# Kernel tuning notes

Measured on AMD Instinct MI355X. Metric: run time of the kernel, lower is better.

The kernel has to match this reference:

```python
import jax, jax.numpy as jnp
import numpy as np
import math

V, D, H, DFF, NL, CTX = 32000, 512, 8, 2048, 2, 1024
B, S = 2, 1024

def ln(x, w, eps=1e-5):
    mu = jnp.mean(x, axis=-1, keepdims=True)
    var = jnp.var(x, axis=-1, keepdims=True)
    return (x - mu) / jnp.sqrt(var + eps) * w

def setup_inputs() -> dict:
    key = jax.random.key(0)
    ks = jax.random.split(key, 10)
    inp = {
        "x": jax.random.randint(ks[0], (B, S), 0, V),
        "wte": jax.random.normal(ks[1], (V, D), jnp.float32) * 0.02,
        "wpe": jax.random.normal(ks[2], (CTX + 1, D), jnp.float32) * 0.02,
        "ln_e_w": jnp.ones((D,), jnp.float32),
        "ln_p_w": jnp.ones((D,), jnp.float32),
        "ln_f_w": jnp.ones((D,), jnp.float32),
        "ln_mlp_w": jnp.ones((D,), jnp.float32),
        "W_q_diag": jax.random.normal(ks[3], (H, D), jnp.float32) * 0.02,
        "W_k_diag": jax.random.normal(ks[4], (H, D), jnp.float32) * 0.02,
        "W_o": jax.random.normal(ks[5], (NL, D, D * H), jnp.float32) * (0.02 / math.sqrt(2 * NL)),
        "mlp_w1": jax.random.normal(ks[6], (DFF, D), jnp.float32) * 0.02,
        "mlp_w2": jax.random.normal(ks[7], (D, DFF), jnp.float32) * 0.02,
    }
    return inp

def reference(x, wte, wpe, ln_e_w, ln_p_w, ln_f_w, ln_mlp_w, W_q_diag, W_k_diag, W_o, mlp_w1, mlp_w2):
    Bsz, Sl = x.shape
    e = ln(wte[x], ln_e_w)                       # (B,S,D)
    p = ln(wpe[: Sl + 1], ln_p_w)                # (S+1,D), identical across batch
    Q = p[1:][None, :, :] * W_q_diag[:, None, :]   # (H,S,D)
    K = p[:-1][None, :, :] * W_k_diag[:, None, :]  # (H,S,D)
    krn = jnp.einsum('hsd,htd->hst', Q, K) / math.sqrt(D)
    mask = jnp.tril(jnp.ones((Sl, Sl), bool))
    krn = jnp.where(mask[None], krn, 0.0)        # (H,S,S)
    wn = 1.0 / (jnp.arange(Sl, dtype=jnp.float32) + 1.0)  # W_N diagonal

    f_k = jnp.zeros_like(e)
    for i in range(NL):
        # R = softmax over S of (V,D)@(B,D,S) -> (B,V,S)
        R = jax.nn.softmax(jnp.einsum('vd,bsd->bvs', wte, f_k), axis=-1)
        ex_wte = jnp.einsum('bvs,vd->bsd', R, wte)
        ex_wte = ex_wte / jnp.sum(R, axis=1)[..., None]  # normalize by sum over V
        Vt = e - ex_wte                                   # (B,S,D)
        delta = jnp.einsum('hst,btd->bhsd', krn, Vt)      # (B,H,S,D)
        delta = delta * wn[None, None, :, None]           # W_N row scaling
        delta = jnp.transpose(delta, (0, 2, 1, 3)).reshape(Bsz, Sl, H * D)
        delta = delta @ W_o[i].T                          # (B,S,D)
        f_k = f_k + delta
        # use_ff MLP block
        h = ln(f_k, ln_mlp_w)
        f_k = f_k + jax.nn.gelu(h @ mlp_w1.T, approximate=False) @ mlp_w2.T

    out = ln(f_k, ln_f_w)
    logits = out[:, -1:, :] @ wte.T               # (B,1,V), targets=None branch
    return logits
```

## Files before the change

kernel.cpp:

```cpp
#include <hip/hip_runtime.h>

#define DV   512
#define SV   1024
#define BV   2
#define VV   32000
#define HV   8
#define DFFV 2048
#define NLV  2
#define KCX  25

typedef __bf16 bf16;
typedef __bf16 bf16x4 __attribute__((ext_vector_type(4)));
typedef __bf16 bf16x8 __attribute__((ext_vector_type(8)));
typedef float  f32x4  __attribute__((ext_vector_type(4)));

__device__ __forceinline__ void lds_dma16(const void* g, void* l) {
  __builtin_amdgcn_global_load_lds(
      (const __attribute__((address_space(1))) unsigned int*)g,
      (__attribute__((address_space(3))) unsigned int*)l,
      16, 0, 0);
}

template<typename OUT>
__device__ __forceinline__ void row_ln_512(const float* __restrict__ src,
                                           const float* __restrict__ w,
                                           OUT* __restrict__ dst, int lane) {
  const float4 a = *(const float4*)(src + lane*8);
  const float4 b = *(const float4*)(src + lane*8 + 4);
  float s = a.x+a.y+a.z+a.w + b.x+b.y+b.z+b.w;
  float q = a.x*a.x+a.y*a.y+a.z*a.z+a.w*a.w + b.x*b.x+b.y*b.y+b.z*b.z+b.w*b.w;
#pragma unroll
  for (int off = 32; off > 0; off >>= 1) {
    s += __shfl_down(s, off, 64);
    q += __shfl_down(q, off, 64);
  }
  s = __shfl(s, 0, 64); q = __shfl(q, 0, 64);
  const float mu   = s * (1.0f/512.0f);
  const float rstd = rsqrtf(q * (1.0f/512.0f) - mu*mu + 1e-5f);
  const float4 wa = *(const float4*)(w + lane*8);
  const float4 wb = *(const float4*)(w + lane*8 + 4);
  OUT* d = dst + lane*8;
  d[0] = (OUT)((a.x-mu)*rstd*wa.x);
  d[1] = (OUT)((a.y-mu)*rstd*wa.y);
  d[2] = (OUT)((a.z-mu)*rstd*wa.z);
  d[3] = (OUT)((a.w-mu)*rstd*wa.w);
  d[4] = (OUT)((b.x-mu)*rstd*wb.x);
  d[5] = (OUT)((b.y-mu)*rstd*wb.y);
  d[6] = (OUT)((b.z-mu)*rstd*wb.z);
  d[7] = (OUT)((b.w-mu)*rstd*wb.w);
}

__global__ void embed_wpe_ln_k(const int* __restrict__ x, const float* __restrict__ wte,
                               const float* __restrict__ wpe, const float* __restrict__ we,
                               const float* __restrict__ wp, float* __restrict__ e,
                               float* __restrict__ pn) {
  const int row = blockIdx.x * 4 + (threadIdx.x >> 6);
  const int lane = threadIdx.x & 63;
  if (row < BV*SV) {
    row_ln_512<float>(wte + (long)x[row] * DV, we, e + (long)row * DV, lane);
  } else {
    const int r = row - BV*SV;
    if (r >= SV + 1) return;
    row_ln_512<float>(wpe + (long)r * DV, wp, pn + (long)r * DV, lane);
  }
}

__global__ void cast3_f2b_k(const float* __restrict__ Wo, const float* __restrict__ w1,
                            const float* __restrict__ w2, bf16* __restrict__ Wob,
                            bf16* __restrict__ w1b, bf16* __restrict__ w2b) {
  const long n0 = (long)NLV*DV*HV*DV, n1 = (long)DFFV*DV, n2 = (long)DV*DFFV;
  long i = ((long)blockIdx.x * 256 + threadIdx.x) * 4;
  const float* in; bf16* o; long r;
  if (i < n0)            { in = Wo; o = Wob; r = i; }
  else if (i < n0 + n1)  { in = w1; o = w1b; r = i - n0; }
  else if (i < n0+n1+n2) { in = w2; o = w2b; r = i - n0 - n1; }
  else return;
  const float4 v = *(const float4*)(in + r);
  bf16x4 ob; ob[0]=(bf16)v.x; ob[1]=(bf16)v.y; ob[2]=(bf16)v.z; ob[3]=(bf16)v.w;
  *(bf16x4*)(&o[r]) = ob;
}

__global__ void wte_prep_k(const float* __restrict__ wte, bf16* __restrict__ wb,
                           bf16* __restrict__ wbT, float* __restrict__ wm) {
  __shared__ float t[32][33];
  __shared__ float cpart[8][32];
  const int d0 = blockIdx.x * 32, v0 = blockIdx.y * 32;
  const int tx = threadIdx.x, ty = threadIdx.y;
  float csum = 0.f;
#pragma unroll
  for (int k = 0; k < 4; k++) {
    const int vl = ty*4 + k;
    const float val = wte[(long)(v0+vl)*DV + d0+tx];
    t[vl][tx] = val;
    csum += val;
  }
  cpart[ty][tx] = csum;
  __syncthreads();
  const int tid = ty*32 + tx;
  const int r = tid >> 3, c = (tid & 7) * 4;
  {
    bf16x4 o;
    o[0] = (bf16)t[r][c];   o[1] = (bf16)t[r][c+1];
    o[2] = (bf16)t[r][c+2]; o[3] = (bf16)t[r][c+3];
    *(bf16x4*)(&wb[(long)(v0+r)*DV + d0+c]) = o;
  }
  {
    bf16x4 o;
    o[0] = (bf16)t[c][r];   o[1] = (bf16)t[c+1][r];
    o[2] = (bf16)t[c+2][r]; o[3] = (bf16)t[c+3][r];
    *(bf16x4*)(&wbT[(long)(d0+r)*VV + v0+c]) = o;
  }
  if (ty == 0) {
    float s = 0.f;
#pragma unroll
    for (int k = 0; k < 8; k++) s += cpart[k][tx];
    atomicAdd(&wm[d0+tx], s);
  }
}

__global__ void qk_prep_k(const float* __restrict__ pn, const float* __restrict__ Wq,
                          const float* __restrict__ Wk, bf16* __restrict__ Qh,
                          bf16* __restrict__ Kh) {
  const int s = blockIdx.x, hh = blockIdx.y;
  const int d = threadIdx.x * 4;
  const float4 q  = *(const float4*)(pn + (long)(s+1)*DV + d);
  const float4 kk = *(const float4*)(pn + (long)s*DV + d);
  const float4 aq = *(const float4*)(Wq + (long)hh*DV + d);
  const float4 ak = *(const float4*)(Wk + (long)hh*DV + d);
  const long o = ((long)hh*SV + s)*DV + d;
  Qh[o+0]=(bf16)(q.x*aq.x);  Qh[o+1]=(bf16)(q.y*aq.y);
  Qh[o+2]=(bf16)(q.z*aq.z);  Qh[o+3]=(bf16)(q.w*aq.w);
  Kh[o+0]=(bf16)(kk.x*ak.x); Kh[o+1]=(bf16)(kk.y*ak.y);
  Kh[o+2]=(bf16)(kk.z*ak.z); Kh[o+3]=(bf16)(kk.w*ak.w);
}

__global__ void freduce_ln_k(const float* __restrict__ part, float* __restrict__ f_k,
                             const float* __restrict__ w, bf16* __restrict__ hbuf,
                             int KC, int init) {
  const int row = blockIdx.x * 4 + (threadIdx.x >> 6);
  const int lane = threadIdx.x & 63;
  const int b = row >> 10;
  const long ro = (long)row * DV + lane*8;
  const long po = (long)(row & (SV-1)) * DV + lane*8;
  float v[8];
  if (init) {
#pragma unroll
    for (int k = 0; k < 8; k++) v[k] = 0.f;
  } else {
    const float4 a = *(const float4*)(f_k + ro);
    const float4 c = *(const float4*)(f_k + ro + 4);
    v[0]=a.x;v[1]=a.y;v[2]=a.z;v[3]=a.w;v[4]=c.x;v[5]=c.y;v[6]=c.z;v[7]=c.w;
  }
  for (int c = 0; c < KC; c++) {
    const float* pp = part + ((long)(b*KC + c))*SV*DV + po;
    const float4 a = *(const float4*)pp;
    const float4 d = *(const float4*)(pp + 4);
    v[0]+=a.x;v[1]+=a.y;v[2]+=a.z;v[3]+=a.w;v[4]+=d.x;v[5]+=d.y;v[6]+=d.z;v[7]+=d.w;
  }
  { float4 o1={v[0],v[1],v[2],v[3]}, o2={v[4],v[5],v[6],v[7]};
    *(float4*)(f_k + ro) = o1; *(float4*)(f_k + ro + 4) = o2; }
  float s = 0.f, q = 0.f;
#pragma unroll
  for (int k = 0; k < 8; k++) { s += v[k]; q += v[k]*v[k]; }
#pragma unroll
  for (int off = 32; off > 0; off >>= 1) {
    s += __shfl_down(s, off, 64);
    q += __shfl_down(q, off, 64);
  }
  s = __shfl(s, 0, 64); q = __shfl(q, 0, 64);
  const float mu   = s * (1.0f/512.0f);
  const float rstd = rsqrtf(q * (1.0f/512.0f) - mu*mu + 1e-5f);
  const float4 wa = *(const float4*)(w + lane*8);
  const float4 wb = *(const float4*)(w + lane*8 + 4);
  bf16* d = hbuf + (long)row * DV + lane*8;
  d[0] = (bf16)((v[0]-mu)*rstd*wa.x);
  d[1] = (bf16)((v[1]-mu)*rstd*wa.y);
  d[2] = (bf16)((v[2]-mu)*rstd*wa.z);
  d[3] = (bf16)((v[3]-mu)*rstd*wa.w);
  d[4] = (bf16)((v[4]-mu)*rstd*wb.x);
  d[5] = (bf16)((v[5]-mu)*rstd*wb.y);
  d[6] = (bf16)((v[6]-mu)*rstd*wb.z);
  d[7] = (bf16)((v[7]-mu)*rstd*wb.w);
}

__global__ void freduce_cast_k(const float* __restrict__ part, float* __restrict__ f_k,
                               bf16* __restrict__ fb, int KC, int do_cast) {
  const long i = ((long)blockIdx.x * 256 + threadIdx.x) * 4;
  const int  b = (int)(i / ((long)SV*DV));
  const long r = i % ((long)SV*DV);
  float4 acc = *(const float4*)(f_k + i);
  for (int c = 0; c < KC; c++) {
    const float4 v = *(const float4*)(part + ((long)(b*KC + c))*SV*DV + r);
    acc.x += v.x; acc.y += v.y; acc.z += v.z; acc.w += v.w;
  }
  *(float4*)(f_k + i) = acc;
  if (do_cast) {
    bf16x4 o; o[0]=(bf16)acc.x; o[1]=(bf16)acc.y; o[2]=(bf16)acc.z; o[3]=(bf16)acc.w;
    *(bf16x4*)(&fb[i]) = o;
  }
}

__global__ void vt_part_k(const float* __restrict__ e, const bf16* __restrict__ pb,
                          const float* __restrict__ part, bf16* __restrict__ VtT) {
  __shared__ float t[32][33];
  __shared__ float cpart[8][32];
  __shared__ float csum[32];
  const int d0 = blockIdx.x * 32, s0 = blockIdx.y * 32;
  const int tx = threadIdx.x, ty = threadIdx.y;
  {
    float cs = 0.f;
    for (int v = ty; v < VV/128; v += 8) cs += part[(long)v * SV + s0 + tx];
    cpart[ty][tx] = cs;
  }
  __syncthreads();
  if (ty == 0) {
    float s = 0.f;
#pragma unroll
    for (int k = 0; k < 8; k++) s += cpart[k][tx];
    csum[tx] = s;
  }
  __syncthreads();
#pragma unroll
  for (int k = 0; k < 4; k++) {
    const int sl = ty + k*8;
    const long off = (long)(s0+sl)*DV + d0+tx;
    float acc = 0.f;
    for (int c = 0; c < KCX; c++) acc += (float)pb[(long)c*SV*DV + off];
    t[sl][tx] = e[off] - acc / csum[sl];
  }
  __syncthreads();
#pragma unroll
  for (int k = 0; k < 4; k++) {
    const int dl = ty + k*8;
    VtT[(long)(d0+dl)*SV + s0+tx] = (bf16)t[tx][dl];
  }
}

__global__ void vt0_transpose_k(const float* __restrict__ e, const float* __restrict__ wm,
                                bf16* __restrict__ VtT) {
  __shared__ float t[32][33];
  const int d0 = blockIdx.x * 32, s0 = blockIdx.y * 32, b = blockIdx.z;
  const int tx = threadIdx.x, ty = threadIdx.y;
  const float* eb = e + (long)b*SV*DV;
  bf16* vb = VtT + (long)b*DV*SV;
  const float mval = wm[d0 + tx] * (1.0f / (float)VV);
#pragma unroll
  for (int k = 0; k < 4; k++) {
    const int sl = ty + k*8;
    t[sl][tx] = eb[(long)(s0+sl)*DV + d0+tx] - mval;
  }
  __syncthreads();
#pragma unroll
  for (int k = 0; k < 4; k++) {
    const int dl = ty + k*8;
    vb[(long)(d0+dl)*SV + s0+tx] = (bf16)t[tx][dl];
  }
}


__global__ void u_last_k(const bf16* __restrict__ krn, const bf16* __restrict__ VtT,
                         bf16* __restrict__ u) {
  const int wv = threadIdx.x >> 6, lane = threadIdx.x & 63;
  const int d = blockIdx.x * 4 + wv;
  const int h = blockIdx.y, b = blockIdx.z;
  const bf16* kr = krn + (long)h*SV*SV + (long)(SV-1)*SV;
  const bf16* vr = VtT + (long)b*DV*SV + (long)d*SV;
  float acc = 0.f;
#pragma unroll
  for (int it = 0; it < 2; it++) {
    const int k = lane*8 + it*512;
    const bf16x8 a = *(const bf16x8*)(kr + k);
    const bf16x8 v = *(const bf16x8*)(vr + k);
#pragma unroll
    for (int i = 0; i < 8; i++) acc += (float)a[i] * (float)v[i];
  }
#pragma unroll
  for (int off = 32; off > 0; off >>= 1) acc += __shfl_down(acc, off, 64);
  if (lane == 0) u[((long)b*HV + h)*DV + d] = (bf16)acc;
}

template<int ACT>
__global__ void gemv_k(const bf16* __restrict__ W, const bf16* __restrict__ vec,
                       float* __restrict__ outf, bf16* __restrict__ outb,
                       int M, int K, long sVb) {
  const int wv = threadIdx.x >> 6, lane = threadIdx.x & 63;
  const int m = blockIdx.x * 4 + wv;
  const int b = blockIdx.y;
  if (m >= M) return;
  const bf16* wr = W + (long)m * K;
  const bf16* vb = vec + (long)b * sVb;
  float acc = 0.f;
  for (int k = lane*8; k < K; k += 512) {
    const bf16x8 a = *(const bf16x8*)(wr + k);
    const bf16x8 v = *(const bf16x8*)(vb + k);
#pragma unroll
    for (int i = 0; i < 8; i++) acc += (float)a[i] * (float)v[i];
  }
#pragma unroll
  for (int off = 32; off > 0; off >>= 1) acc += __shfl_down(acc, off, 64);
  if (lane == 0) {
    if (ACT == 0) outf[(long)b * M + m] = acc;
    else {
      const float ge = 0.5f * acc * (1.0f + erff(acc * 0.70710678118f));
      outb[(long)b * M + m] = (bf16)ge;
    }
  }
}

__global__ void mid_ln_k(const float* __restrict__ f_k, const float* __restrict__ delta,
                         const float* __restrict__ w, float* __restrict__ f_last,
                         bf16* __restrict__ h) {
  const int b = threadIdx.x >> 6;
  if (b >= BV) return;
  const int lane = threadIdx.x & 63;
  const long ro = ((long)b * SV + (SV - 1)) * DV + lane*8;
  const float* dp = delta + (long)b * DV + lane*8;
  float v[8];
  { const float4 a = *(const float4*)(f_k + ro);
    const float4 c = *(const float4*)(f_k + ro + 4);
    const float4 da = *(const float4*)dp;
    const float4 db = *(const float4*)(dp + 4);
    v[0]=a.x+da.x; v[1]=a.y+da.y; v[2]=a.z+da.z; v[3]=a.w+da.w;
    v[4]=c.x+db.x; v[5]=c.y+db.y; v[6]=c.z+db.z; v[7]=c.w+db.w; }
  { float* fl = f_last + (long)b*DV + lane*8;
    float4 o1={v[0],v[1],v[2],v[3]}, o2v={v[4],v[5],v[6],v[7]};
    *(float4*)fl = o1; *(float4*)(fl+4) = o2v; }
  float s = 0.f, q = 0.f;
#pragma unroll
  for (int k = 0; k < 8; k++) { s += v[k]; q += v[k]*v[k]; }
#pragma unroll
  for (int off = 32; off > 0; off >>= 1) {
    s += __shfl_down(s, off, 64);
    q += __shfl_down(q, off, 64);
  }
  s = __shfl(s, 0, 64); q = __shfl(q, 0, 64);
  const float mu   = s * (1.0f/512.0f);
  const float rstd = rsqrtf(q * (1.0f/512.0f) - mu*mu + 1e-5f);
  const float4 wa = *(const float4*)(w + lane*8);
  const float4 wb = *(const float4*)(w + lane*8 + 4);
  bf16* d = h + (long)b * DV + lane*8;
  d[0] = (bf16)((v[0]-mu)*rstd*wa.x);
  d[1] = (bf16)((v[1]-mu)*rstd*wa.y);
  d[2] = (bf16)((v[2]-mu)*rstd*wa.z);
  d[3] = (bf16)((v[3]-mu)*rstd*wa.w);
  d[4] = (bf16)((v[4]-mu)*rstd*wb.x);
  d[5] = (bf16)((v[5]-mu)*rstd*wb.y);
  d[6] = (bf16)((v[6]-mu)*rstd*wb.z);
  d[7] = (bf16)((v[7]-mu)*rstd*wb.w);
}

__global__ void final2_k(const float* __restrict__ f_last, const float* __restrict__ o2,
                         const float* __restrict__ w, float* __restrict__ obuf) {
  const int b = threadIdx.x >> 6;
  if (b >= BV) return;
  const int lane = threadIdx.x & 63;
  const float* fl = f_last + (long)b * DV + lane*8;
  const float* op = o2 + (long)b * DV + lane*8;
  float v[8];
  { const float4 a = *(const float4*)fl;
    const float4 c = *(const float4*)(fl + 4);
    const float4 da = *(const float4*)op;
    const float4 db = *(const float4*)(op + 4);
    v[0]=a.x+da.x; v[1]=a.y+da.y; v[2]=a.z+da.z; v[3]=a.w+da.w;
    v[4]=c.x+db.x; v[5]=c.y+db.y; v[6]=c.z+db.z; v[7]=c.w+db.w; }
  float s = 0.f, q = 0.f;
#pragma unroll
  for (int k = 0; k < 8; k++) { s += v[k]; q += v[k]*v[k]; }
#pragma unroll
  for (int off = 32; off > 0; off >>= 1) {
    s += __shfl_down(s, off, 64);
    q += __shfl_down(q, off, 64);
  }
  s = __shfl(s, 0, 64); q = __shfl(q, 0, 64);
  const float mu   = s * (1.0f/512.0f);
  const float rstd = rsqrtf(q * (1.0f/512.0f) - mu*mu + 1e-5f);
  const float4 wa = *(const float4*)(w + lane*8);
  const float4 wb = *(const float4*)(w + lane*8 + 4);
  float* d = obuf + (long)b * DV + lane*8;
  d[0] = (v[0]-mu)*rstd*wa.x;
  d[1] = (v[1]-mu)*rstd*wa.y;
  d[2] = (v[2]-mu)*rstd*wa.z;
  d[3] = (v[3]-mu)*rstd*wa.w;
  d[4] = (v[4]-mu)*rstd*wb.x;
  d[5] = (v[5]-mu)*rstd*wb.y;
  d[6] = (v[6]-mu)*rstd*wb.z;
  d[7] = (v[7]-mu)*rstd*wb.w;
}

__global__ void logits_k(const float* __restrict__ obuf, const float* __restrict__ wte,
                         float* __restrict__ out, int V) {
  const int wv = threadIdx.x >> 6, lane = threadIdx.x & 63;
  const int v = blockIdx.x * 4 + wv;
  const float* wr = wte + (long)v * DV;
  const float4 a  = *(const float4*)(wr + lane*8);
  const float4 c  = *(const float4*)(wr + lane*8 + 4);
  const float4 oa0 = *(const float4*)(obuf + lane*8);
  const float4 ob0 = *(const float4*)(obuf + lane*8 + 4);
  const float4 oa1 = *(const float4*)(obuf + DV + lane*8);
  const float4 ob1 = *(const float4*)(obuf + DV + lane*8 + 4);
  float d0 = a.x*oa0.x + a.y*oa0.y + a.z*oa0.z + a.w*oa0.w
           + c.x*ob0.x + c.y*ob0.y + c.z*ob0.z + c.w*ob0.w;
  float d1 = a.x*oa1.x + a.y*oa1.y + a.z*oa1.z + a.w*oa1.w
           + c.x*ob1.x + c.y*ob1.y + c.z*ob1.z + c.w*ob1.w;
#pragma unroll
  for (int off = 32; off > 0; off >>= 1) {
    d0 += __shfl_down(d0, off, 64);
    d1 += __shfl_down(d1, off, 64);
  }
  if (lane == 0) { out[v] = d0; out[(long)V + v] = d1; }
}

__device__ __forceinline__ long xcd_swz(long lin, long nwg) {
  const long qq = nwg >> 3, rr = nwg & 7;
  const long xcd = lin & 7, idx = lin >> 3;
  return (xcd < rr ? xcd * (qq + 1) : rr * (qq + 1) + (xcd - rr) * qq) + idx;
}

struct GemmArgs {
  const bf16* A; const bf16* B;
  float* Cf; bf16* Cb;
  int K, lda, ldb, ldc;
  long sAh, sAb, sBh, sBb, sCh, sCb;
  int Hmod, KC, causal, swap;
  float scale;
};

template<int EPI>
__global__ __launch_bounds__(256)
void gemm_nt(GemmArgs g) {
  __shared__ bf16 As[2][128*32];
  __shared__ bf16 Bs[2][128*32];
  const int tid = threadIdx.x;
  int bx = blockIdx.x, by = blockIdx.y, z = blockIdx.z;
  {
    const int nbx = gridDim.x, nby = gridDim.y;
    const long nwg = (long)nbx * nby * gridDim.z;
    long lin = xcd_swz(bx + (long)nbx * (by + (long)nby * z), nwg);
    bx = (int)(lin % nbx);
    const long t2 = lin / nbx;
    by = (int)(t2 % nby);
    z  = (int)(t2 / nby);
  }
  const int chunk = z % g.KC;
  const int zo = z / g.KC;
  const int h = zo % g.Hmod;
  const int b = zo / g.Hmod;
  if (g.swap) { int t = bx; bx = by; by = t; }
  const int m0 = by * 128;
  const int n0 = bx * 128;
  const long coff = (long)h * g.sCh + (long)b * g.sCb;

  if (EPI == 3 && n0 > m0 + 127) return;

  const bf16* A = g.A + (long)h * g.sAh + (long)b * g.sAb;
  const bf16* B = g.B + (long)h * g.sBh + (long)b * g.sBb;
  const int lane = tid & 63;
  const int wv = tid >> 6;
  const int wm = (wv >> 1) * 64;
  const int wn = (wv & 1) * 64;
  const int frow = lane & 15;
  const int quad = lane >> 4;
  const int sg8  = ((lane & 3) ^ ((lane >> 3) & 3)) * 8;
  const int drow = lane >> 2;

  const f32x4 fzero = {0.f, 0.f, 0.f, 0.f};
  f32x4 acc[4][4];
#pragma unroll
  for (int i = 0; i < 4; i++)
#pragma unroll
    for (int j = 0; j < 4; j++) acc[i][j] = fzero;

  int k0, klen;
  if (g.causal) { k0 = 0; klen = min(g.K, m0 + 128); }
  else          { klen = g.K / g.KC; k0 = chunk * klen; }

  auto stage = [&](int buf, int kk) {
#pragma unroll
    for (int c = 0; c < 2; c++) {
      const int rb = c*64 + wv*16;
      lds_dma16(A + (long)(m0 + rb + drow) * g.lda + kk + sg8, &As[buf][rb*32]);
      lds_dma16(B + (long)(n0 + rb + drow) * g.ldb + kk + sg8, &Bs[buf][rb*32]);
    }
  };

  const int nsteps = klen >> 5;
  int cur = 0;
  stage(0, k0);
  for (int it = 0; it < nsteps; ++it) {
    if (it + 1 < nsteps) {
      stage(cur ^ 1, k0 + (it + 1) * 32);
      asm volatile("s_waitcnt vmcnt(4)" ::: "memory");
    } else {
      asm volatile("s_waitcnt vmcnt(0)" ::: "memory");
    }
    __builtin_amdgcn_s_barrier();
    bf16x8 af[4], bfr[4];
    const int sw = (frow >> 1) & 3;
#pragma unroll
    for (int i = 0; i < 4; i++)
      af[i] = *(const bf16x8*)(&As[cur][(wm + i*16 + frow)*32 + ((quad ^ sw))*8]);
#pragma unroll
    for (int j = 0; j < 4; j++)
      bfr[j] = *(const bf16x8*)(&Bs[cur][(wn + j*16 + frow)*32 + ((quad ^ sw))*8]);
#pragma unroll
    for (int i = 0; i < 4; i++)
#pragma unroll
      for (int j = 0; j < 4; j++)
        acc[i][j] = __builtin_amdgcn_mfma_f32_16x16x32_bf16(af[i], bfr[j], acc[i][j], 0, 0, 0);
    __builtin_amdgcn_s_barrier();
    cur ^= 1;
  }

  const int rb = quad * 4;
#pragma unroll
  for (int i = 0; i < 4; i++) {
#pragma unroll
    for (int j = 0; j < 4; j++) {
#pragma unroll
      for (int r = 0; r < 4; r++) {
        const int gm = m0 + wm + i*16 + rb + r;
        const int gn = n0 + wn + j*16 + frow;
        const float v = acc[i][j][r];
        if (EPI == 2) {
          g.Cb[coff + (long)gm * g.ldc + gn] = (bf16)v;
        } else if (EPI == 3) {
          const float val = (gn <= gm) ? v * g.scale / (float)(gm + 1) : 0.0f;
          g.Cb[coff + (long)gm * g.ldc + gn] = (bf16)val;
        } else if (EPI == 4) {
          const float ge = 0.5f * v * (1.0f + erff(v * 0.70710678118f));
          g.Cb[coff + (long)gm * g.ldc + gn] = (bf16)ge;
        } else if (EPI == 6) {
          g.Cf[(long)(b*g.KC + chunk) * g.sCh + (long)gm * g.ldc + gn] = v;
        }
      }
    }
  }
}

template<int EPI>
__global__ __launch_bounds__(512)
void gemm256(GemmArgs g) {
  __shared__ bf16 As[2][256*64];
  __shared__ bf16 Bs[2][256*64];
  const int tid = threadIdx.x;
  int bm = blockIdx.x, bn = blockIdx.y, z = blockIdx.z;
  {
    const int nbx = gridDim.x, nby = gridDim.y;
    const long nwg = (long)nbx * nby * gridDim.z;
    long lin = xcd_swz(bm + (long)nbx * (bn + (long)nby * z), nwg);
    bm = (int)(lin % nbx);
    const long t2 = lin / nbx;
    bn = (int)(t2 % nby);
    z  = (int)(t2 / nby);
  }
  const int m0 = bm * 256, n0 = bn * 256;
  const int lane = tid & 63, wv = tid >> 6;
  const int wm = (wv >> 2) * 128, wn = (wv & 3) * 64;
  const int frow = lane & 15, quad = lane >> 4;
  const int sg8  = ((lane & 7) ^ (lane >> 3)) * 8;
  const int drow = lane >> 3;

  const f32x4 fzero = {0.f, 0.f, 0.f, 0.f};
  f32x4 acc[8][4];
#pragma unroll
  for (int i = 0; i < 8; i++)
#pragma unroll
    for (int j = 0; j < 4; j++) acc[i][j] = fzero;

  const int klen = g.K / g.KC;
  const int k0 = z * klen;

  auto stage = [&](int buf, int kk) {
#pragma unroll
    for (int c = 0; c < 4; c++) {
      const int rb = c*64 + wv*8;
      lds_dma16(g.A + (long)(m0 + rb + drow) * g.lda + kk + sg8, &As[buf][rb*64]);
      lds_dma16(g.B + (long)(n0 + rb + drow) * g.ldb + kk + sg8, &Bs[buf][rb*64]);
    }
  };

  const int nsteps = klen >> 6;
  int cur = 0;
  stage(0, k0);
  for (int it = 0; it < nsteps; ++it) {
    if (it + 1 < nsteps) {
      stage(cur ^ 1, k0 + (it + 1) * 64);
      asm volatile("s_waitcnt vmcnt(8)" ::: "memory");
    } else {
      asm volatile("s_waitcnt vmcnt(0)" ::: "memory");
    }
    __builtin_amdgcn_s_barrier();
    const int sw = frow & 7;
#pragma unroll
    for (int ks = 0; ks < 2; ks++) {
      bf16x8 af[8], bfr[4];
#pragma unroll
      for (int j = 0; j < 4; j++)
        bfr[j] = *(const bf16x8*)(&Bs[cur][(wn + j*16 + frow)*64 + (((ks*4 + quad) ^ sw))*8]);
#pragma unroll
      for (int i = 0; i < 8; i++)
        af[i] = *(const bf16x8*)(&As[cur][(wm + i*16 + frow)*64 + (((ks*4 + quad) ^ sw))*8]);
#pragma unroll
      for (int i = 0; i < 8; i++)
#pragma unroll
        for (int j = 0; j < 4; j++)
          acc[i][j] = __builtin_amdgcn_mfma_f32_16x16x32_bf16(af[i], bfr[j], acc[i][j], 0, 0, 0);
    }
    __builtin_amdgcn_s_barrier();
    cur ^= 1;
  }

  const int rb4 = quad * 4;
  if (EPI == 5) {
    const int vblk = (n0 + wn) >> 7;
#pragma unroll
    for (int i = 0; i < 8; i++) {
#pragma unroll
      for (int r = 0; r < 4; r++) {
        const int gm = m0 + wm + i*16 + rb4 + r;
        float rs = 0.f;
#pragma unroll
        for (int j = 0; j < 4; j++) {
          const int gn = n0 + wn + j*16 + frow;
          const float ev = __expf(acc[i][j][r]);
          g.Cb[(long)gm * g.ldc + gn] = (bf16)ev;
          rs += ev;
        }
#pragma unroll
        for (int off = 1; off < 16; off <<= 1)
          rs += __shfl_xor(rs, off, 64);
        if (frow == 0) atomicAdd(g.Cf + (long)vblk * SV + gm, rs);
      }
    }
  } else {
#pragma unroll
    for (int i = 0; i < 8; i++) {
#pragma unroll
      for (int j = 0; j < 4; j++) {
#pragma unroll
        for (int r = 0; r < 4; r++) {
          const int gm = m0 + wm + i*16 + rb4 + r;
          const int gn = n0 + wn + j*16 + frow;
          g.Cb[(long)z * g.sCh + (long)gm * g.ldc + gn] = (bf16)acc[i][j][r];
        }
      }
    }
  }
}

static void layer_tail0(bf16* krn, bf16* VtT, bf16* U_rs, bf16* Wo_b,
                        float* f_k, bf16* f_k_b, bf16* hbuf, bf16* Gbuf, float* fpart,
                        bf16* w1_b, bf16* w2_b, const float* lnmw, hipStream_t stream) {
  {
    GemmArgs g = {};
    g.A = krn; g.B = VtT; g.Cb = U_rs;
    g.K = SV; g.lda = SV; g.ldb = SV; g.ldc = HV*DV;
    g.sAh = (long)SV*SV; g.sBb = (long)DV*SV;
    g.sCh = DV; g.sCb = (long)SV*HV*DV;
    g.Hmod = HV; g.KC = 1; g.causal = 1;
    gemm_nt<2><<<dim3(DV/128, SV/128, BV*HV), 256, 0, stream>>>(g);
  }
  {
    GemmArgs g = {};
    g.A = U_rs; g.B = Wo_b; g.Cf = fpart;
    g.K = HV*DV; g.lda = HV*DV; g.ldb = HV*DV; g.ldc = DV;
    g.sAb = (long)SV*HV*DV; g.sCh = (long)SV*DV;
    g.Hmod = 1; g.KC = 8; g.causal = 0;
    gemm_nt<6><<<dim3(DV/128, SV/128, BV*8), 256, 0, stream>>>(g);
  }
  freduce_ln_k<<<dim3(BV*SV/4), 256, 0, stream>>>(fpart, f_k, lnmw, hbuf, 8, 1);
  {
    GemmArgs g = {};
    g.A = hbuf; g.B = w1_b; g.Cb = Gbuf;
    g.K = DV; g.lda = DV; g.ldb = DV; g.ldc = DFFV;
    g.sAb = (long)SV*DV; g.sCb = (long)SV*DFFV;
    g.Hmod = 1; g.KC = 1; g.causal = 0;
    gemm_nt<4><<<dim3(DFFV/128, SV/128, BV), 256, 0, stream>>>(g);
  }
  {
    GemmArgs g = {};
    g.A = Gbuf; g.B = w2_b; g.Cf = fpart;
    g.K = DFFV; g.lda = DFFV; g.ldb = DFFV; g.ldc = DV;
    g.sAb = (long)SV*DFFV; g.sCh = (long)SV*DV;
    g.Hmod = 1; g.KC = 8; g.causal = 0;
    gemm_nt<6><<<dim3(DV/128, SV/128, BV*8), 256, 0, stream>>>(g);
  }
  freduce_cast_k<<<dim3(BV*SV*DV/4/256), 256, 0, stream>>>(fpart, f_k, f_k_b, 8, 1);
}

extern "C" void kernel_launch(void* const* d_in, const int* in_sizes, int n_in,
                              void* d_out, int out_size, void* d_ws, size_t ws_size,
                              hipStream_t stream) {
  const int*   x    = (const int*)d_in[0];
  const float* wte  = (const float*)d_in[1];
  const float* wpe  = (const float*)d_in[2];
  const float* lnew = (const float*)d_in[3];
  const float* lnpw = (const float*)d_in[4];
  const float* lnfw = (const float*)d_in[5];
  const float* lnmw = (const float*)d_in[6];
  const float* Wq   = (const float*)d_in[7];
  const float* Wk   = (const float*)d_in[8];
  const float* Wo   = (const float*)d_in[9];
  const float* w1   = (const float*)d_in[10];
  const float* w2   = (const float*)d_in[11];
  float* out = (float*)d_out;
  (void)in_sizes; (void)n_in; (void)out_size; (void)ws_size;

  char* p = (char*)d_ws;
  auto alloc = [&](size_t bytes) -> void* {
    void* r = (void*)p;
    p += (bytes + 255) & ~(size_t)255;
    return r;
  };
  float* e      = (float*)alloc((size_t)BV*SV*DV*4);
  float* pn     = (float*)alloc((size_t)(SV+1)*DV*4);
  bf16*  wteT_b = (bf16*)alloc((size_t)DV*VV*2);
  bf16*  wte_b  = (bf16*)alloc((size_t)VV*DV*2);
  bf16*  krn    = (bf16*)alloc((size_t)HV*SV*SV*2);
  bf16*  Wo_b   = (bf16*)alloc((size_t)NLV*DV*HV*DV*2);
  bf16*  w1_b   = (bf16*)alloc((size_t)DFFV*DV*2);
  bf16*  w2_b   = (bf16*)alloc((size_t)DV*DFFV*2);
  float* f_k    = (float*)alloc((size_t)BV*SV*DV*4);
  bf16*  f_k_b  = (bf16*)alloc((size_t)BV*SV*DV*2);
  bf16*  expart = (bf16*)alloc((size_t)KCX*SV*DV*2);
  bf16*  VtT    = (bf16*)alloc((size_t)BV*DV*SV*2);
  bf16*  hbuf   = (bf16*)alloc((size_t)BV*SV*DV*2);
  float* part   = (float*)alloc((size_t)BV*(VV/128)*SV*4);
  float* obuf   = (float*)alloc((size_t)BV*DV*4);
  float* wmean  = (float*)alloc((size_t)DV*4);
  bf16*  u_last = (bf16*)alloc((size_t)BV*HV*DV*2);
  float* delta  = (float*)alloc((size_t)BV*DV*4);
  float* f_last = (float*)alloc((size_t)BV*DV*4);
  bf16*  h_last = (bf16*)alloc((size_t)BV*DV*2);
  bf16*  g_last = (bf16*)alloc((size_t)BV*DFFV*2);
  float* o2buf  = (float*)alloc((size_t)BV*DV*4);
  char*  arena  = (char*)alloc((size_t)SV*VV*2);
  bf16*  Qh     = (bf16*)arena;
  bf16*  Kh     = (bf16*)(arena + (size_t)HV*SV*DV*2);
  bf16*  PT     = (bf16*)arena;
  bf16*  U_rs   = (bf16*)arena;
  bf16*  Gbuf   = (bf16*)(arena + (size_t)BV*SV*HV*DV*2);
  float* fpart  = (float*)(arena + (size_t)BV*SV*HV*DV*2 + (size_t)BV*SV*DFFV*2);

  hipMemsetAsync(wmean, 0, (size_t)DV*4, stream);
  hipMemsetAsync(part, 0, (size_t)BV*(VV/128)*SV*4, stream);
  wte_prep_k<<<dim3(DV/32, VV/32), dim3(32,8), 0, stream>>>(wte, wte_b, wteT_b, wmean);
  cast3_f2b_k<<<dim3((NLV*DV*HV*DV + DFFV*DV + DV*DFFV)/4/256), 256, 0, stream>>>(
      Wo, w1, w2, Wo_b, w1_b, w2_b);
  embed_wpe_ln_k<<<dim3((BV*SV + SV+1 + 3)/4), 256, 0, stream>>>(
      x, wte, wpe, lnew, lnpw, e, pn);
  qk_prep_k<<<dim3(SV, HV), 128, 0, stream>>>(pn, Wq, Wk, Qh, Kh);

  {
    GemmArgs g = {};
    g.A = Qh; g.B = Kh; g.Cb = krn;
    g.K = DV; g.lda = DV; g.ldb = DV; g.ldc = SV;
    g.sAh = (long)SV*DV; g.sBh = (long)SV*DV; g.sCh = (long)SV*SV;
    g.Hmod = HV; g.KC = 1; g.causal = 0;
    g.scale = 0.044194173824159216f;
    gemm_nt<3><<<dim3(SV/128, SV/128, HV), 256, 0, stream>>>(g);
  }

  vt0_transpose_k<<<dim3(DV/32, SV/32, BV), dim3(32,8), 0, stream>>>(e, wmean, VtT);
  layer_tail0(krn, VtT, U_rs, Wo_b, f_k, f_k_b, hbuf, Gbuf, fpart,
              w1_b, w2_b, lnmw, stream);

  for (int b = 0; b < BV; b++) {
    float* partb = part + (long)b*(VV/128)*SV;
    {
      GemmArgs g = {};
      g.A = f_k_b + (long)b*SV*DV; g.B = wte_b; g.Cb = PT; g.Cf = partb;
      g.K = DV; g.lda = DV; g.ldb = DV; g.ldc = VV;
      g.KC = 1;
      gemm256<5><<<dim3(SV/256, VV/256, 1), 512, 0, stream>>>(g);
    }
    {
      GemmArgs g = {};
      g.A = PT; g.B = wteT_b; g.Cb = expart;
      g.K = VV; g.lda = VV; g.ldb = VV; g.ldc = DV;
      g.sCh = (long)SV*DV;
      g.KC = KCX;
      gemm256<7><<<dim3(SV/256, DV/256, KCX), 512, 0, stream>>>(g);
    }
    vt_part_k<<<dim3(DV/32, SV/32), dim3(32,8), 0, stream>>>(
        e + (long)b*SV*DV, expart, partb, VtT + (long)b*DV*SV);
  }

  u_last_k<<<dim3(DV/4, HV, BV), 256, 0, stream>>>(krn, VtT, u_last);
  gemv_k<0><<<dim3(DV/4, BV), 256, 0, stream>>>(
      Wo_b + (long)1*DV*HV*DV, u_last, delta, nullptr, DV, HV*DV, (long)HV*DV);
  mid_ln_k<<<1, 128, 0, stream>>>(f_k, delta, lnmw, f_last, h_last);
  gemv_k<1><<<dim3(DFFV/4, BV), 256, 0, stream>>>(
      w1_b, h_last, nullptr, g_last, DFFV, DV, (long)DV);
  gemv_k<0><<<dim3(DV/4, BV), 256, 0, stream>>>(
      w2_b, g_last, o2buf, nullptr, DV, DFFV, (long)DFFV);
  final2_k<<<1, 128, 0, stream>>>(f_last, o2buf, lnfw, obuf);
  logits_k<<<dim3(VV/4), 256, 0, stream>>>(obuf, wte, out, VV);
}
```

Baseline: 438.1 us.

## Compute second-layer attention only for the last row via reassociated softmax expectation

The final layer's output is needed only at the last position, so the full (S x V) by (V x D) expectation GEMM and the Vt transpose are replaced by a reassociated path. The path weights the probabilities by the last krn row divided by column sums to get q (H x V), then contracts q with wte, plus a separate krn·e term. This removes the large K=32000 GEMM, the transposed wte copy and the expart partial-sum buffer. In exchange it adds several simple scalar kernels with atomics, which are less efficient per FLOP.

```diff
diff --git a/kernel.cpp b/kernel.cpp
--- a/kernel.cpp
+++ b/kernel.cpp
@@ -7,7 +7,6 @@
 #define HV   8
 #define DFFV 2048
 #define NLV  2
-#define KCX  25
 
 typedef __bf16 bf16;
 typedef __bf16 bf16x4 __attribute__((ext_vector_type(4)));
@@ -81,8 +80,7 @@
 }
 
 __global__ void wte_prep_k(const float* __restrict__ wte, bf16* __restrict__ wb,
-                           bf16* __restrict__ wbT, float* __restrict__ wm) {
-  __shared__ float t[32][33];
+                           float* __restrict__ wm) {
   __shared__ float cpart[8][32];
   const int d0 = blockIdx.x * 32, v0 = blockIdx.y * 32;
   const int tx = threadIdx.x, ty = threadIdx.y;
@@ -91,25 +89,11 @@
   for (int k = 0; k < 4; k++) {
     const int vl = ty*4 + k;
     const float val = wte[(long)(v0+vl)*DV + d0+tx];
-    t[vl][tx] = val;
     csum += val;
+    wb[(long)(v0+vl)*DV + d0+tx] = (bf16)val;
   }
   cpart[ty][tx] = csum;
   __syncthreads();
-  const int tid = ty*32 + tx;
-  const int r = tid >> 3, c = (tid & 7) * 4;
-  {
-    bf16x4 o;
-    o[0] = (bf16)t[r][c];   o[1] = (bf16)t[r][c+1];
-    o[2] = (bf16)t[r][c+2]; o[3] = (bf16)t[r][c+3];
-    *(bf16x4*)(&wb[(long)(v0+r)*DV + d0+c]) = o;
-  }
-  {
-    bf16x4 o;
-    o[0] = (bf16)t[c][r];   o[1] = (bf16)t[c+1][r];
-    o[2] = (bf16)t[c+2][r]; o[3] = (bf16)t[c+3][r];
-    *(bf16x4*)(&wbT[(long)(d0+r)*VV + v0+c]) = o;
-  }
   if (ty == 0) {
     float s = 0.f;
 #pragma unroll
@@ -134,6 +118,13 @@
   Kh[o+2]=(bf16)(kk.z*ak.z); Kh[o+3]=(bf16)(kk.w*ak.w);
 }
 
+__global__ void colsum_k(const float* __restrict__ part, float* __restrict__ cs) {
+  const int s = blockIdx.x * 256 + threadIdx.x;
+  float acc = 0.f;
+  for (int v = 0; v < VV/128; v++) acc += part[(long)v * SV + s];
+  cs[s] = acc;
+}
+
 __global__ void freduce_ln_k(const float* __restrict__ part, float* __restrict__ f_k,
                              const float* __restrict__ w, bf16* __restrict__ hbuf,
                              int KC, int init) {
@@ -184,7 +175,7 @@
 }
 
 __global__ void freduce_cast_k(const float* __restrict__ part, float* __restrict__ f_k,
-                               bf16* __restrict__ fb, int KC, int do_cast) {
+                               bf16* __restrict__ fb, int KC) {
   const long i = ((long)blockIdx.x * 256 + threadIdx.x) * 4;
   const int  b = (int)(i / ((long)SV*DV));
   const long r = i % ((long)SV*DV);
@@ -194,46 +185,8 @@
     acc.x += v.x; acc.y += v.y; acc.z += v.z; acc.w += v.w;
   }
   *(float4*)(f_k + i) = acc;
-  if (do_cast) {
-    bf16x4 o; o[0]=(bf16)acc.x; o[1]=(bf16)acc.y; o[2]=(bf16)acc.z; o[3]=(bf16)acc.w;
-    *(bf16x4*)(&fb[i]) = o;
-  }
-}
-
-__global__ void vt_part_k(const float* __restrict__ e, const bf16* __restrict__ pb,
-                          const float* __restrict__ part, bf16* __restrict__ VtT) {
-  __shared__ float t[32][33];
-  __shared__ float cpart[8][32];
-  __shared__ float csum[32];
-  const int d0 = blockIdx.x * 32, s0 = blockIdx.y * 32;
-  const int tx = threadIdx.x, ty = threadIdx.y;
-  {
-    float cs = 0.f;
-    for (int v = ty; v < VV/128; v += 8) cs += part[(long)v * SV + s0 + tx];
-    cpart[ty][tx] = cs;
-  }
-  __syncthreads();
-  if (ty == 0) {
-    float s = 0.f;
-#pragma unroll
-    for (int k = 0; k < 8; k++) s += cpart[k][tx];
-    csum[tx] = s;
-  }
-  __syncthreads();
-#pragma unroll
-  for (int k = 0; k < 4; k++) {
-    const int sl = ty + k*8;
-    const long off = (long)(s0+sl)*DV + d0+tx;
-    float acc = 0.f;
-    for (int c = 0; c < KCX; c++) acc += (float)pb[(long)c*SV*DV + off];
-    t[sl][tx] = e[off] - acc / csum[sl];
-  }
-  __syncthreads();
-#pragma unroll
-  for (int k = 0; k < 4; k++) {
-    const int dl = ty + k*8;
-    VtT[(long)(d0+dl)*SV + s0+tx] = (bf16)t[tx][dl];
-  }
+  bf16x4 o; o[0]=(bf16)acc.x; o[1]=(bf16)acc.y; o[2]=(bf16)acc.z; o[3]=(bf16)acc.w;
+  *(bf16x4*)(&fb[i]) = o;
 }
 
 __global__ void vt0_transpose_k(const float* __restrict__ e, const float* __restrict__ wm,
@@ -258,25 +211,83 @@
 }
 
 
-__global__ void u_last_k(const bf16* __restrict__ krn, const bf16* __restrict__ VtT,
-                         bf16* __restrict__ u) {
-  const int wv = threadIdx.x >> 6, lane = threadIdx.x & 63;
-  const int d = blockIdx.x * 4 + wv;
-  const int h = blockIdx.y, b = blockIdx.z;
-  const bf16* kr = krn + (long)h*SV*SV + (long)(SV-1)*SV;
-  const bf16* vr = VtT + (long)b*DV*SV + (long)d*SV;
-  float acc = 0.f;
-#pragma unroll
-  for (int it = 0; it < 2; it++) {
-    const int k = lane*8 + it*512;
-    const bf16x8 a = *(const bf16x8*)(kr + k);
-    const bf16x8 v = *(const bf16x8*)(vr + k);
-#pragma unroll
-    for (int i = 0; i < 8; i++) acc += (float)a[i] * (float)v[i];
-  }
-#pragma unroll
-  for (int off = 32; off > 0; off >>= 1) acc += __shfl_down(acc, off, 64);
-  if (lane == 0) u[((long)b*HV + h)*DV + d] = (bf16)acc;
+__global__ __launch_bounds__(256) void q_k(const bf16* __restrict__ krn,
+                                           const float* __restrict__ cs,
+                                           const bf16* __restrict__ PT,
+                                           float* __restrict__ q) {
+  __shared__ float kw[HV][SV];
+  const int tid = threadIdx.x;
+  const int v = blockIdx.x * 256 + tid;
+  for (int i = tid; i < HV*SV; i += 256) {
+    const int h = i >> 10, t = i & (SV-1);
+    kw[h][t] = (float)krn[(long)h*SV*SV + (long)(SV-1)*SV + t] / cs[t];
+  }
+  __syncthreads();
+  float acc[HV];
+#pragma unroll
+  for (int h = 0; h < HV; h++) acc[h] = 0.f;
+  for (int t = 0; t < SV; ++t) {
+    const float pv = (float)PT[(long)t*VV + v];
+#pragma unroll
+    for (int h = 0; h < HV; h++) acc[h] += kw[h][t] * pv;
+  }
+#pragma unroll
+  for (int h = 0; h < HV; h++) q[(long)h*VV + v] = acc[h];
+}
+
+__global__ __launch_bounds__(512) void ue_k(const bf16* __restrict__ krn,
+                                            const float* __restrict__ e,
+                                            float* __restrict__ Uacc) {
+  __shared__ float kr[HV][64];
+  const int b = blockIdx.y, t0 = blockIdx.x * 64;
+  const int tid = threadIdx.x;
+  for (int i = tid; i < HV*64; i += 512) {
+    const int h = i >> 6, t = i & 63;
+    kr[h][t] = (float)krn[(long)h*SV*SV + (long)(SV-1)*SV + t0 + t];
+  }
+  __syncthreads();
+  float acc[HV];
+#pragma unroll
+  for (int h = 0; h < HV; h++) acc[h] = 0.f;
+  const float* eb = e + (long)b*SV*DV;
+  for (int t = 0; t < 64; ++t) {
+    const float ev = eb[(long)(t0+t)*DV + tid];
+#pragma unroll
+    for (int h = 0; h < HV; h++) acc[h] += kr[h][t] * ev;
+  }
+  float* ub = Uacc + (long)b*HV*DV;
+#pragma unroll
+  for (int h = 0; h < HV; h++) atomicAdd(&ub[h*DV + tid], acc[h]);
+}
+
+__global__ __launch_bounds__(512) void qw_k(const float* __restrict__ q,
+                                            const bf16* __restrict__ wte_b,
+                                            float* __restrict__ Uacc) {
+  __shared__ float qs[HV][1280];
+  const int b = blockIdx.y, v0 = blockIdx.x * 1280;
+  const int tid = threadIdx.x;
+  const float* qb = q + (long)b*HV*VV;
+  for (int i = tid; i < HV*1280; i += 512) {
+    const int h = i / 1280, v = i - h*1280;
+    qs[h][v] = qb[(long)h*VV + v0 + v];
+  }
+  __syncthreads();
+  float acc[HV];
+#pragma unroll
+  for (int h = 0; h < HV; h++) acc[h] = 0.f;
+  for (int v = 0; v < 1280; ++v) {
+    const float wv = (float)wte_b[(long)(v0+v)*DV + tid];
+#pragma unroll
+    for (int h = 0; h < HV; h++) acc[h] += qs[h][v] * wv;
+  }
+  float* ub = Uacc + (long)b*HV*DV;
+#pragma unroll
+  for (int h = 0; h < HV; h++) atomicAdd(&ub[h*DV + tid], -acc[h]);
+}
+
+__global__ void u_cast_k(const float* __restrict__ Uacc, bf16* __restrict__ u) {
+  const long i = (long)blockIdx.x * 256 + threadIdx.x;
+  u[i] = (bf16)Uacc[i];
 }
 
 template<int ACT>
@@ -611,39 +622,24 @@
   }
 
   const int rb4 = quad * 4;
-  if (EPI == 5) {
-    const int vblk = (n0 + wn) >> 7;
-#pragma unroll
-    for (int i = 0; i < 8; i++) {
-#pragma unroll
-      for (int r = 0; r < 4; r++) {
-        const int gm = m0 + wm + i*16 + rb4 + r;
-        float rs = 0.f;
-#pragma unroll
-        for (int j = 0; j < 4; j++) {
-          const int gn = n0 + wn + j*16 + frow;
-          const float ev = __expf(acc[i][j][r]);
-          g.Cb[(long)gm * g.ldc + gn] = (bf16)ev;
-          rs += ev;
-        }
-#pragma unroll
-        for (int off = 1; off < 16; off <<= 1)
-          rs += __shfl_xor(rs, off, 64);
-        if (frow == 0) atomicAdd(g.Cf + (long)vblk * SV + gm, rs);
+  const int vblk = (n0 + wn) >> 7;
+#pragma unroll
+  for (int i = 0; i < 8; i++) {
+#pragma unroll
+    for (int r = 0; r < 4; r++) {
+      const int gm = m0 + wm + i*16 + rb4 + r;
+      float rs = 0.f;
+#pragma unroll
+      for (int j = 0; j < 4; j++) {
+        const int gn = n0 + wn + j*16 + frow;
+        const float ev = __expf(acc[i][j][r]);
+        g.Cb[(long)gm * g.ldc + gn] = (bf16)ev;
+        rs += ev;
       }
-    }
-  } else {
-#pragma unroll
-    for (int i = 0; i < 8; i++) {
-#pragma unroll
-      for (int j = 0; j < 4; j++) {
-#pragma unroll
-        for (int r = 0; r < 4; r++) {
-          const int gm = m0 + wm + i*16 + rb4 + r;
-          const int gn = n0 + wn + j*16 + frow;
-          g.Cb[(long)z * g.sCh + (long)gm * g.ldc + gn] = (bf16)acc[i][j][r];
-        }
-      }
+#pragma unroll
+      for (int off = 1; off < 16; off <<= 1)
+        rs += __shfl_xor(rs, off, 64);
+      if (frow == 0) atomicAdd(g.Cf + (long)vblk * SV + gm, rs);
     }
   }
 }
@@ -685,7 +681,7 @@
     g.Hmod = 1; g.KC = 8; g.causal = 0;
     gemm_nt<6><<<dim3(DV/128, SV/128, BV*8), 256, 0, stream>>>(g);
   }
-  freduce_cast_k<<<dim3(BV*SV*DV/4/256), 256, 0, stream>>>(fpart, f_k, f_k_b, 8, 1);
+  freduce_cast_k<<<dim3(BV*SV*DV/4/256), 256, 0, stream>>>(fpart, f_k, f_k_b, 8);
 }
 
 extern "C" void kernel_launch(void* const* d_in, const int* in_sizes, int n_in,
@@ -714,7 +710,6 @@
   };
   float* e      = (float*)alloc((size_t)BV*SV*DV*4);
   float* pn     = (float*)alloc((size_t)(SV+1)*DV*4);
-  bf16*  wteT_b = (bf16*)alloc((size_t)DV*VV*2);
   bf16*  wte_b  = (bf16*)alloc((size_t)VV*DV*2);
   bf16*  krn    = (bf16*)alloc((size_t)HV*SV*SV*2);
   bf16*  Wo_b   = (bf16*)alloc((size_t)NLV*DV*HV*DV*2);
@@ -722,10 +717,12 @@
   bf16*  w2_b   = (bf16*)alloc((size_t)DV*DFFV*2);
   float* f_k    = (float*)alloc((size_t)BV*SV*DV*4);
   bf16*  f_k_b  = (bf16*)alloc((size_t)BV*SV*DV*2);
-  bf16*  expart = (bf16*)alloc((size_t)KCX*SV*DV*2);
   bf16*  VtT    = (bf16*)alloc((size_t)BV*DV*SV*2);
   bf16*  hbuf   = (bf16*)alloc((size_t)BV*SV*DV*2);
   float* part   = (float*)alloc((size_t)BV*(VV/128)*SV*4);
+  float* csum   = (float*)alloc((size_t)BV*SV*4);
+  float* qbuf   = (float*)alloc((size_t)BV*HV*VV*4);
+  float* Uacc   = (float*)alloc((size_t)BV*HV*DV*4);
   float* obuf   = (float*)alloc((size_t)BV*DV*4);
   float* wmean  = (float*)alloc((size_t)DV*4);
   bf16*  u_last = (bf16*)alloc((size_t)BV*HV*DV*2);
@@ -744,7 +741,8 @@
 
   hipMemsetAsync(wmean, 0, (size_t)DV*4, stream);
   hipMemsetAsync(part, 0, (size_t)BV*(VV/128)*SV*4, stream);
-  wte_prep_k<<<dim3(DV/32, VV/32), dim3(32,8), 0, stream>>>(wte, wte_b, wteT_b, wmean);
+  hipMemsetAsync(Uacc, 0, (size_t)BV*HV*DV*4, stream);
+  wte_prep_k<<<dim3(DV/32, VV/32), dim3(32,8), 0, stream>>>(wte, wte_b, wmean);
   cast3_f2b_k<<<dim3((NLV*DV*HV*DV + DFFV*DV + DV*DFFV)/4/256), 256, 0, stream>>>(
       Wo, w1, w2, Wo_b, w1_b, w2_b);
   embed_wpe_ln_k<<<dim3((BV*SV + SV+1 + 3)/4), 256, 0, stream>>>(
@@ -760,6 +758,7 @@
     g.scale = 0.044194173824159216f;
     gemm_nt<3><<<dim3(SV/128, SV/128, HV), 256, 0, stream>>>(g);
   }
+  ue_k<<<dim3(SV/64, BV), 512, 0, stream>>>(krn, e, Uacc);
 
   vt0_transpose_k<<<dim3(DV/32, SV/32, BV), dim3(32,8), 0, stream>>>(e, wmean, VtT);
   layer_tail0(krn, VtT, U_rs, Wo_b, f_k, f_k_b, hbuf, Gbuf, fpart,
@@ -774,19 +773,13 @@
       g.KC = 1;
       gemm256<5><<<dim3(SV/256, VV/256, 1), 512, 0, stream>>>(g);
     }
-    {
-      GemmArgs g = {};
-      g.A = PT; g.B = wteT_b; g.Cb = expart;
-      g.K = VV; g.lda = VV; g.ldb = VV; g.ldc = DV;
-      g.sCh = (long)SV*DV;
-      g.KC = KCX;
-      gemm256<7><<<dim3(SV/256, DV/256, KCX), 512, 0, stream>>>(g);
-    }
-    vt_part_k<<<dim3(DV/32, SV/32), dim3(32,8), 0, stream>>>(
-        e + (long)b*SV*DV, expart, partb, VtT + (long)b*DV*SV);
-  }
-
-  u_last_k<<<dim3(DV/4, HV, BV), 256, 0, stream>>>(krn, VtT, u_last);
+    colsum_k<<<dim3(SV/256), 256, 0, stream>>>(partb, csum + (long)b*SV);
+    q_k<<<dim3(VV/256), 256, 0, stream>>>(krn, csum + (long)b*SV, PT,
+                                          qbuf + (long)b*HV*VV);
+  }
+  qw_k<<<dim3(VV/1280, BV), 512, 0, stream>>>(qbuf, wte_b, Uacc);
+  u_cast_k<<<dim3(BV*HV*DV/256), 256, 0, stream>>>(Uacc, u_last);
+
   gemv_k<0><<<dim3(DV/4, BV), 256, 0, stream>>>(
       Wo_b + (long)1*DV*HV*DV, u_last, delta, nullptr, DV, HV*DV, (long)HV*DV);
   mid_ln_k<<<1, 128, 0, stream>>>(f_k, delta, lnmw, f_last, h_last);
```

Result: slower. 647.6 us (+47.8%).
